# Optimization experiments

Measured on AMD Instinct MI355X. Metric: run time of the kernel, lower is better.

Reference implementation:

```python
import jax, jax.numpy as jnp
import numpy as np

IN_CHANNELS = 64
NY, NX = 496, 432
N_VOXELS = 64000
BATCH = 4


def setup_inputs() -> dict:
    key = jax.random.key(0)
    k1, k2, k3, k4 = jax.random.split(key, 4)
    voxel_features = jax.random.normal(k1, (N_VOXELS, IN_CHANNELS), dtype=jnp.float32)
    b = jax.random.randint(k2, (N_VOXELS,), 0, BATCH, dtype=jnp.int32)
    y = jax.random.randint(k3, (N_VOXELS,), 0, NY, dtype=jnp.int32)
    x = jax.random.randint(k4, (N_VOXELS,), 0, NX, dtype=jnp.int32)
    z = jnp.zeros((N_VOXELS,), dtype=jnp.int32)
    coors = jnp.stack([b, z, y, x], axis=1)  # (N, 4): [batch, z, y, x]
    return {"voxel_features": voxel_features, "coors": coors, "batch_size": BATCH}


def reference(voxel_features, coors, batch_size):
    # Fused scatter: flat index into (batch * ny * nx) canvas, single .at[].set.
    # Original overwrites on duplicate coords; pillar coords are unique by construction.
    C = voxel_features.shape[1]
    flat_idx = (coors[:, 0].astype(jnp.int32) * (NY * NX)
                + coors[:, 2].astype(jnp.int32) * NX
                + coors[:, 3].astype(jnp.int32))  # (N,)
    canvas = jnp.zeros((batch_size * NY * NX, C), dtype=voxel_features.dtype)
    canvas = canvas.at[flat_idx].set(voxel_features)
    # (B*ny*nx, C) -> (B, C, ny, nx)
    canvas = canvas.reshape(batch_size, NY, NX, C).transpose(0, 3, 1, 2)
    return canvas
```

## Files before the change

kernel.cpp:

```cpp
#include <hip/hip_runtime.h>


#define C_CH 64
#define NY_ 496
#define NX_ 432
#define NPIX (NY_ * NX_)
#define NVOX 64000
#define BATCH_ 4
#define PIX4 (NPIX / 4)

typedef float f32x4 __attribute__((ext_vector_type(4)));

__global__ void pps_winners(const int* __restrict__ coors, int* __restrict__ ws) {
    int i = blockIdx.x * blockDim.x + threadIdx.x;
    if (i >= NVOX) return;
    const int4 cv = reinterpret_cast<const int4*>(coors)[i];
    atomicMax(&ws[cv.x * NPIX + cv.z * NX_ + cv.w], i);
}

__global__ void __launch_bounds__(256) pps_gather(const float* __restrict__ vf,
                                                  const int* __restrict__ ws,
                                                  float* __restrict__ out) {
    int wg = (blockIdx.x & 7) * (53568 / 8) + (blockIdx.x >> 3);
    int tid = wg * 256 + threadIdx.x;

    int bc = tid / PIX4;
    int p4 = tid - bc * PIX4;
    int b = bc >> 6;
    int c = bc & 63;
    int pix = p4 * 4;

    const int4 w = *reinterpret_cast<const int4*>(&ws[b * NPIX + pix]);
    f32x4 o;
    o.x = (w.x >= 0) ? vf[(long)w.x * C_CH + c] : 0.0f;
    o.y = (w.y >= 0) ? vf[(long)w.y * C_CH + c] : 0.0f;
    o.z = (w.z >= 0) ? vf[(long)w.z * C_CH + c] : 0.0f;
    o.w = (w.w >= 0) ? vf[(long)w.w * C_CH + c] : 0.0f;

    *reinterpret_cast<f32x4*>(&out[(long)bc * NPIX + pix]) = o;
}

extern "C" void kernel_launch(void* const* d_in, const int* in_sizes, int n_in,
                              void* d_out, int out_size, void* d_ws, size_t ws_size,
                              hipStream_t stream) {
    const float* vf = (const float*)d_in[0];
    const int* coors = (const int*)d_in[1];
    float* out = (float*)d_out;
    int* ws = (int*)d_ws;

    (void)hipMemsetAsync(ws, 0xFF, (size_t)BATCH_ * NPIX * sizeof(int), stream);

    pps_winners<<<(NVOX + 255) / 256, 256, 0, stream>>>(coors, ws);

    pps_gather<<<BATCH_ * C_CH * PIX4 / 256, 256, 0, stream>>>(vf, ws, out);
}
```

Measured before the change: 241.7 us.

## Gather 16 channels per thread with vector loads and nontemporal scalar stores

Each thread now handles one pixel and a group of 16 channels. It reads the winner index once, loads 64 contiguous bytes of features with vector loads, and writes 16 channel planes using nontemporal stores. The goal is to cut repeated winner-index reads and scattered per-channel feature gathers, and to stop the large output from polluting the cache. The trade-off is that stores become scalar 4-byte writes (still coalesced across the wave) instead of 16-byte vector stores, and each thread needs more registers.

```diff
diff --git a/kernel.cpp b/kernel.cpp
--- a/kernel.cpp
+++ b/kernel.cpp
@@ -7,7 +7,8 @@
 #define NPIX (NY_ * NX_)
 #define NVOX 64000
 #define BATCH_ 4
-#define PIX4 (NPIX / 4)
+#define PBLK 837
+#define NWG (BATCH_ * 4 * PBLK)
 
 typedef float f32x4 __attribute__((ext_vector_type(4)));
 
@@ -21,23 +22,40 @@
 __global__ void __launch_bounds__(256) pps_gather(const float* __restrict__ vf,
                                                   const int* __restrict__ ws,
                                                   float* __restrict__ out) {
-    int wg = (blockIdx.x & 7) * (53568 / 8) + (blockIdx.x >> 3);
-    int tid = wg * 256 + threadIdx.x;
+    int bid = blockIdx.x;
+    int wg = (bid & 7) * (NWG / 8) + (bid >> 3);
 
-    int bc = tid / PIX4;
-    int p4 = tid - bc * PIX4;
-    int b = bc >> 6;
-    int c = bc & 63;
-    int pix = p4 * 4;
+    int blk = wg % PBLK;
+    int bcg = wg / PBLK;
+    int cg = bcg & 3;
+    int b = bcg >> 2;
 
-    const int4 w = *reinterpret_cast<const int4*>(&ws[b * NPIX + pix]);
-    f32x4 o;
-    o.x = (w.x >= 0) ? vf[(long)w.x * C_CH + c] : 0.0f;
-    o.y = (w.y >= 0) ? vf[(long)w.y * C_CH + c] : 0.0f;
-    o.z = (w.z >= 0) ? vf[(long)w.z * C_CH + c] : 0.0f;
-    o.w = (w.w >= 0) ? vf[(long)w.w * C_CH + c] : 0.0f;
+    int pix = blk * 256 + threadIdx.x;
+    int w = ws[b * NPIX + pix];
 
-    *reinterpret_cast<f32x4*>(&out[(long)bc * NPIX + pix]) = o;
+    f32x4 v0 = {0.f, 0.f, 0.f, 0.f}, v1 = v0, v2 = v0, v3 = v0;
+    if (w >= 0) {
+        const f32x4* src = reinterpret_cast<const f32x4*>(vf + (long)w * C_CH + cg * 16);
+        v0 = src[0]; v1 = src[1]; v2 = src[2]; v3 = src[3];
+    }
+
+    float* o = out + ((long)(b * C_CH + cg * 16)) * NPIX + pix;
+    __builtin_nontemporal_store(v0.x, o);
+    __builtin_nontemporal_store(v0.y, o + 1L * NPIX);
+    __builtin_nontemporal_store(v0.z, o + 2L * NPIX);
+    __builtin_nontemporal_store(v0.w, o + 3L * NPIX);
+    __builtin_nontemporal_store(v1.x, o + 4L * NPIX);
+    __builtin_nontemporal_store(v1.y, o + 5L * NPIX);
+    __builtin_nontemporal_store(v1.z, o + 6L * NPIX);
+    __builtin_nontemporal_store(v1.w, o + 7L * NPIX);
+    __builtin_nontemporal_store(v2.x, o + 8L * NPIX);
+    __builtin_nontemporal_store(v2.y, o + 9L * NPIX);
+    __builtin_nontemporal_store(v2.z, o + 10L * NPIX);
+    __builtin_nontemporal_store(v2.w, o + 11L * NPIX);
+    __builtin_nontemporal_store(v3.x, o + 12L * NPIX);
+    __builtin_nontemporal_store(v3.y, o + 13L * NPIX);
+    __builtin_nontemporal_store(v3.z, o + 14L * NPIX);
+    __builtin_nontemporal_store(v3.w, o + 15L * NPIX);
 }
 
 extern "C" void kernel_launch(void* const* d_in, const int* in_sizes, int n_in,
@@ -52,5 +70,5 @@
 
     pps_winners<<<(NVOX + 255) / 256, 256, 0, stream>>>(coors, ws);
 
-    pps_gather<<<BATCH_ * C_CH * PIX4 / 256, 256, 0, stream>>>(vf, ws, out);
+    pps_gather<<<NWG, 256, 0, stream>>>(vf, ws, out);
 }
```

Result: no change. 241.7 us (-0.0%).
